# Kernel tuning notes

Measured on AMD Instinct MI355X. Metric: run time of the kernel, lower is better.

## Reference

```python
import jax, jax.numpy as jnp
import numpy as np

IN_CH = 512
HID = 512
SCALE = 1.0 / np.sqrt(16.0)  # hard-coded 16**0.5 in source, not sqrt(hidden)


def setup_inputs() -> dict:
    key = jax.random.key(0)
    ks = jax.random.split(key, 9)
    B, T = 8, 2048
    lim = 1.0 / np.sqrt(IN_CH)
    return {
        "q": jax.random.normal(ks[0], (B, T, IN_CH), dtype=jnp.float32),
        "k": jax.random.normal(ks[1], (B, T, IN_CH), dtype=jnp.float32),
        "v": jax.random.normal(ks[2], (B, T, IN_CH), dtype=jnp.float32),
        "Wq": jax.random.uniform(ks[3], (IN_CH, HID), jnp.float32, -lim, lim),
        "bq": jax.random.uniform(ks[4], (HID,), jnp.float32, -lim, lim),
        "Wk": jax.random.uniform(ks[5], (IN_CH, HID), jnp.float32, -lim, lim),
        "bk": jax.random.uniform(ks[6], (HID,), jnp.float32, -lim, lim),
        "Wv": jax.random.uniform(ks[7], (IN_CH, HID), jnp.float32, -lim, lim),
        "bv": jax.random.uniform(ks[8], (HID,), jnp.float32, -lim, lim),
    }


def reference(q, k, v, Wq, bq, Wk, bk, Wv, bv):
    # Linear projections: [B,T,F] @ [F,H] + [H]
    query = jnp.einsum("btf,fh->bth", q, Wq) + bq
    key_p = jnp.einsum("btf,fh->bth", k, Wk) + bk
    value = jnp.einsum("btf,fh->bth", v, Wv) + bv
    # energy: [B,T,T], scaled by fixed 1/sqrt(16)
    energy = jnp.einsum("bth,bsh->bts", query, key_p) * SCALE
    attn = jax.nn.softmax(energy, axis=-1)
    # weighted sum: [B,T,H]
    return jnp.einsum("bts,bsh->bth", attn, value)
```

## Files before the change

### kernel.cpp

```cpp
#include <hip/hip_runtime.h>
#include <stdint.h>

typedef __bf16 bf16;
typedef bf16 bf16x8 __attribute__((ext_vector_type(8)));
typedef float f32x4 __attribute__((ext_vector_type(4)));

#define MFMA(a, b, c) __builtin_amdgcn_mfma_f32_16x16x32_bf16(a, b, c, 0, 0, 0)

#define SCALE_L2E 0.3606737602222409f
#define M0 16.0f

#define WAITVM(N) asm volatile("s_waitcnt vmcnt(" #N ")" ::: "memory")
#define WAITLGKM0 asm volatile("s_waitcnt lgkmcnt(0)" ::: "memory")
#define SBAR __builtin_amdgcn_s_barrier()
#define SCHEDB __builtin_amdgcn_sched_barrier(0)
#define PRIO(x) __builtin_amdgcn_s_setprio(x)

__device__ __forceinline__ void gload_lds16(const void* g, void* l) {
  __builtin_amdgcn_global_load_lds(
      (const __attribute__((address_space(1))) uint32_t*)g,
      (__attribute__((address_space(3))) uint32_t*)l, 16, 0, 0);
}

__global__ void k_wtrans(const float* __restrict__ Wq, const float* __restrict__ Wk,
                         const float* __restrict__ Wv, bf16* __restrict__ Wt) {
  __shared__ float tile[32][33];
  int x = threadIdx.x, y = threadIdx.y;
  int k0 = blockIdx.x * 32, n0 = blockIdx.y * 32, z = blockIdx.z;
  const float* W = (z == 0) ? Wq : (z == 1) ? Wk : Wv;
  for (int j = 0; j < 4; j++)
    tile[y + 8 * j][x] = W[(size_t)(k0 + y + 8 * j) * 512 + n0 + x];
  __syncthreads();
  bf16* o = Wt + (size_t)z * 262144;
  for (int j = 0; j < 4; j++)
    o[(size_t)(n0 + y + 8 * j) * 512 + k0 + x] = (bf16)tile[x][y + 8 * j];
}

__global__ __launch_bounds__(256, 3) void k_proj(
    const float* __restrict__ q, const float* __restrict__ k, const float* __restrict__ v,
    const bf16* __restrict__ Wt, const float* __restrict__ bq, const float* __restrict__ bk,
    const float* __restrict__ bv, bf16* __restrict__ Qp, bf16* __restrict__ Kp,
    bf16* __restrict__ Vtp) {
  int z = blockIdx.z;
  const float* A = (z == 0) ? q : (z == 1) ? k : v;
  const float* bias = (z == 0) ? bq : (z == 1) ? bk : bv;
  const bf16* Bw = Wt + (size_t)z * 262144;

  int m0 = blockIdx.x * 128, n0 = blockIdx.y * 128;
  __shared__ __align__(16) char smem[49152];
  bf16* As = (bf16*)smem;
  bf16* Bs = (bf16*)(smem + 16384);
  bf16* Ts = (bf16*)smem;

  int tid = threadIdx.x;
  int wave = tid >> 6, lane = tid & 63, qr = lane & 15, quad = lane >> 4;
  int wm = (wave >> 1) * 64, wn = (wave & 1) * 64;

  f32x4 acc[4][4];
  for (int mi = 0; mi < 4; mi++)
    for (int ni = 0; ni < 4; ni++) acc[mi][ni] = (f32x4){0.f, 0.f, 0.f, 0.f};

  float4 rxE[4], ryE[4];
  float4 rxO[4], ryO[4];

  auto issueA = [&](int kk, float4 (&rx)[4], float4 (&ry)[4]) {
#pragma unroll
    for (int i = 0; i < 4; i++) {
      int ch = i * 256 + tid, row = ch >> 3, c = ch & 7;
      const float4* src = (const float4*)(A + (size_t)(m0 + row) * 512 + kk + c * 8);
      rx[i] = src[0];
      ry[i] = src[1];
    }
    SCHEDB;
  };

  auto issueB = [&](int kk, int buf) {
#pragma unroll
    for (int i = 0; i < 4; i++) {
      int ch = i * 256 + tid, row = ch >> 3, c = ch & 7, cs = c ^ (row & 7);
      gload_lds16(Bw + (size_t)(n0 + row) * 512 + kk + cs * 8, &Bs[buf * 8192 + ch * 8]);
    }
    SCHEDB;
  };

  auto writeA = [&](float4 (&rx)[4], float4 (&ry)[4]) {
#pragma unroll
    for (int i = 0; i < 4; i++) {
      int ch = i * 256 + tid, row = ch >> 3, c = ch & 7, cs = c ^ (row & 7);
      bf16x8 t;
      t[0] = (bf16)rx[i].x; t[1] = (bf16)rx[i].y; t[2] = (bf16)rx[i].z; t[3] = (bf16)rx[i].w;
      t[4] = (bf16)ry[i].x; t[5] = (bf16)ry[i].y; t[6] = (bf16)ry[i].z; t[7] = (bf16)ry[i].w;
      *(bf16x8*)&As[row * 64 + cs * 8] = t;
    }
  };

  auto compute = [&](int buf) {
    bf16* Bb = &Bs[buf * 8192];
#pragma unroll
    for (int h = 0; h < 2; h++) {
      bf16x8 af[4], bfv[4];
#pragma unroll
      for (int mi = 0; mi < 4; mi++) {
        int rr = wm + mi * 16 + qr;
        int cc = (h * 4 + quad) ^ (rr & 7);
        af[mi] = *(bf16x8*)&As[rr * 64 + cc * 8];
      }
#pragma unroll
      for (int ni = 0; ni < 4; ni++) {
        int rr = wn + ni * 16 + qr;
        int cc = (h * 4 + quad) ^ (rr & 7);
        bfv[ni] = *(bf16x8*)&Bb[rr * 64 + cc * 8];
      }
#pragma unroll
      for (int mi = 0; mi < 4; mi++)
#pragma unroll
        for (int ni = 0; ni < 4; ni++) acc[mi][ni] = MFMA(af[mi], bfv[ni], acc[mi][ni]);
    }
  };

  issueA(0, rxE, ryE);
  issueB(0, 0);
  issueA(64, rxO, ryO);

#pragma unroll
  for (int t = 0; t < 8; t += 2) {
    writeA(rxE, ryE);
    issueB((t + 1) * 64, 1);
    if (t < 6) issueA((t + 2) * 64, rxE, ryE);
    if (t < 6) { WAITVM(20); } else { WAITVM(12); }
    WAITLGKM0;
    SBAR;
    SCHEDB;
    compute(0);
    SBAR;

    int u = t + 1;
    writeA(rxO, ryO);
    if (u < 7) issueB((u + 1) * 64, 0);
    if (u < 6) issueA((u + 2) * 64, rxO, ryO);
    if (u < 6) { WAITVM(20); } else if (u < 7) { WAITVM(12); } else { WAITVM(0); }
    WAITLGKM0;
    SBAR;
    SCHEDB;
    compute(1);
    SBAR;
  }

  if (z == 2) {
    for (int ni = 0; ni < 4; ni++) {
      int hcol = wn + ni * 16 + qr;
      float bz = bias[n0 + hcol];
      for (int mi = 0; mi < 4; mi++) {
        int tl = wm + mi * 16 + quad * 4;
        bf16 tmp[4];
        for (int r = 0; r < 4; r++) tmp[r] = (bf16)(acc[mi][ni][r] + bz);
        *(uint64_t*)&Ts[hcol * 136 + tl] = *(uint64_t*)tmp;
      }
    }
    __syncthreads();
    int bb = m0 >> 11, t0l = m0 & 2047;
    for (int i = 0; i < 8; i++) {
      int ch = i * 256 + tid;
      int row = ch >> 4, c = ch & 15;
      *(bf16x8*)(Vtp + (size_t)(bb * 512 + n0 + row) * 2048 + t0l + c * 8) =
          *(bf16x8*)&Ts[row * 136 + c * 8];
    }
  } else {
    bf16* C = (z == 0) ? Qp : Kp;
    float sc = (z == 0) ? SCALE_L2E : 1.0f;
    for (int ni = 0; ni < 4; ni++) {
      int col = n0 + wn + ni * 16 + qr;
      float bz = bias[col];
      for (int mi = 0; mi < 4; mi++) {
        int rbase = m0 + wm + mi * 16 + quad * 4;
        for (int r = 0; r < 4; r++)
          C[(size_t)(rbase + r) * 512 + col] = (bf16)((acc[mi][ni][r] + bz) * sc);
      }
    }
  }
}

__global__ __launch_bounds__(512, 1) void k_qk(const bf16* __restrict__ Qp,
                                               const bf16* __restrict__ Kp,
                                               bf16* __restrict__ P,
                                               float* __restrict__ Lpart) {
  __shared__ __align__(16) bf16 S[65536];
  int id = blockIdx.x;
  int b = id & 7, j = id >> 3;
  int mx = j & 7, ny = j >> 3;
  const bf16* A = Qp + (size_t)b * 2048 * 512;
  const bf16* B = Kp + (size_t)b * 2048 * 512;
  bf16* Pb = P + (size_t)b * 2048 * 2048;
  int m0 = mx * 256, n0 = ny * 256;
  int tid = threadIdx.x;
  int wave = tid >> 6, lane = tid & 63, qr = lane & 15, quad = lane >> 4;
  int wm = wave >> 2, wn = wave & 3;

  f32x4 acc[8][4];
  for (int mi = 0; mi < 8; mi++)
    for (int ni = 0; ni < 4; ni++) acc[mi][ni] = (f32x4){0.f, 0.f, 0.f, 0.f};

  auto stageAj = [&](int t, int s, int jj) {
    int kk = t * 64;
    bf16* As_ = S + s * 16384;
    int ch = jj * 512 + tid, row = ch >> 3, c = ch & 7, cs = c ^ (row & 7);
    gload_lds16(A + (size_t)(m0 + row) * 512 + kk + cs * 8, As_ + ch * 8);
  };
  auto stage = [&](int t, int s) {
    int kk = t * 64;
    bf16* Bs_ = S + 32768 + s * 16384;
#pragma unroll
    for (int jj = 0; jj < 4; jj++) {
      int ch = jj * 512 + tid, row = ch >> 3, c = ch & 7, cs = c ^ (row & 7);
      gload_lds16(B + (size_t)(n0 + row) * 512 + kk + cs * 8, Bs_ + ch * 8);
    }
    stageAj(t, s, 0);
    stageAj(t, s, 2);
    stageAj(t, s, 1);
    stageAj(t, s, 3);
  };

  stage(0, 0);
  stage(1, 1);

  for (int t = 0; t < 8; t++) {
    int cur = t & 1;
    bf16* As_ = S + cur * 16384;
    bf16* Bs_ = S + 32768 + cur * 16384;

    if (t < 7) { WAITVM(10); } else { WAITVM(2); }
    SBAR;
    bf16x8 aF[4][2], bF[4][2];
#pragma unroll
    for (int mi = 0; mi < 4; mi++)
#pragma unroll
      for (int kk = 0; kk < 2; kk++) {
        int row = wm * 128 + mi * 16 + qr;
        aF[mi][kk] = *(bf16x8*)&As_[row * 64 + ((kk * 4 + quad) ^ (row & 7)) * 8];
      }
#pragma unroll
    for (int ni = 0; ni < 4; ni++)
#pragma unroll
      for (int kk = 0; kk < 2; kk++) {
        int row = wn * 64 + ni * 16 + qr;
        bF[ni][kk] = *(bf16x8*)&Bs_[row * 64 + ((kk * 4 + quad) ^ (row & 7)) * 8];
      }
    WAITLGKM0;
    SCHEDB;
    PRIO(1);
#pragma unroll
    for (int kk = 0; kk < 2; kk++)
#pragma unroll
      for (int mi = 0; mi < 4; mi++)
#pragma unroll
        for (int ni = 0; ni < 4; ni++)
          acc[mi][ni] = MFMA(aF[mi][kk], bF[ni][kk], acc[mi][ni]);
    PRIO(0);

    if (t < 7) { WAITVM(8); } else { WAITVM(0); }
    SBAR;
#pragma unroll
    for (int mi = 0; mi < 4; mi++)
#pragma unroll
      for (int kk = 0; kk < 2; kk++) {
        int row = wm * 128 + 64 + mi * 16 + qr;
        aF[mi][kk] = *(bf16x8*)&As_[row * 64 + ((kk * 4 + quad) ^ (row & 7)) * 8];
      }
    WAITLGKM0;
    SBAR;
    if (t < 6) stage(t + 2, cur);
    SCHEDB;
    PRIO(1);
#pragma unroll
    for (int kk = 0; kk < 2; kk++)
#pragma unroll
      for (int mi = 0; mi < 4; mi++)
#pragma unroll
        for (int ni = 0; ni < 4; ni++)
          acc[4 + mi][ni] = MFMA(aF[mi][kk], bF[ni][kk], acc[4 + mi][ni]);
    PRIO(0);
  }

  int slice = ny * 4 + wn;
  float* Lp = Lpart + (size_t)slice * 16384 + b * 2048;
#pragma unroll
  for (int mi = 0; mi < 8; mi++) {
    int rowb = m0 + wm * 128 + mi * 16 + quad * 4;
#pragma unroll
    for (int r = 0; r < 4; r++) {
      float s = 0.f;
      bf16* prow = Pb + (size_t)(rowb + r) * 2048 + n0 + wn * 64 + qr;
#pragma unroll
      for (int ni = 0; ni < 4; ni++) {
        float e = exp2f(acc[mi][ni][r] - M0);
        prow[ni * 16] = (bf16)e;
        s += e;
      }
      s += __shfl_xor(s, 1);
      s += __shfl_xor(s, 2);
      s += __shfl_xor(s, 4);
      s += __shfl_xor(s, 8);
      if (qr == 0) Lp[rowb + r] = s;
    }
  }
}

__global__ __launch_bounds__(512, 1) void k_pv(const bf16* __restrict__ P,
                                               const bf16* __restrict__ Vtp,
                                               const float* __restrict__ Lpart,
                                               float* __restrict__ out) {
  __shared__ __align__(16) bf16 S[49152];
  int id = blockIdx.x;
  int b = id & 7, j = id >> 3;
  int mx = j & 7, ny = j >> 3;
  const bf16* A = P + (size_t)b * 2048 * 2048;
  const bf16* B = Vtp + (size_t)b * 512 * 2048;
  int m0 = mx * 256, n0 = ny * 128;
  int tid = threadIdx.x;
  int wave = tid >> 6, lane = tid & 63, qr = lane & 15, quad = lane >> 4;
  int wmi = wave >> 1, wni = wave & 1;

  float linv_own = 0.f;
  if (tid < 256) {
    float s = 0.f;
    for (int jj = 0; jj < 32; jj++) s += Lpart[(size_t)jj * 16384 + b * 2048 + m0 + tid];
    linv_own = 1.0f / s;
  }

  f32x4 acc[4][4];
  for (int mi = 0; mi < 4; mi++)
    for (int ni = 0; ni < 4; ni++) acc[mi][ni] = (f32x4){0.f, 0.f, 0.f, 0.f};

  auto stage = [&](int t, int s) {
    int kk = t * 64;
    bf16* As_ = S + s * 16384;
    bf16* Bs_ = S + 32768 + s * 8192;
#pragma unroll
    for (int jj = 0; jj < 4; jj++) {
      int ch = jj * 512 + tid, row = ch >> 3, c = ch & 7, cs = c ^ (row & 7);
      gload_lds16(A + (size_t)(m0 + row) * 2048 + kk + cs * 8, As_ + ch * 8);
    }
#pragma unroll
    for (int jj = 0; jj < 2; jj++) {
      int ch = jj * 512 + tid, row = ch >> 3, c = ch & 7, cs = c ^ (row & 7);
      gload_lds16(B + (size_t)(n0 + row) * 2048 + kk + cs * 8, Bs_ + ch * 8);
    }
  };

  stage(0, 0);
  stage(1, 1);

  for (int t = 0; t < 32; t++) {
    int cur = t & 1;
    bf16* As_ = S + cur * 16384;
    bf16* Bs_ = S + 32768 + cur * 8192;

    if (t < 31) { WAITVM(6); } else { WAITVM(0); }
    SBAR;
    bf16x8 aF[4][2], bF[4][2];
#pragma unroll
    for (int mi = 0; mi < 4; mi++)
#pragma unroll
      for (int kk = 0; kk < 2; kk++) {
        int row = wmi * 64 + mi * 16 + qr;
        aF[mi][kk] = *(bf16x8*)&As_[row * 64 + ((kk * 4 + quad) ^ (row & 7)) * 8];
      }
#pragma unroll
    for (int ni = 0; ni < 4; ni++)
#pragma unroll
      for (int kk = 0; kk < 2; kk++) {
        int row = wni * 64 + ni * 16 + qr;
        bF[ni][kk] = *(bf16x8*)&Bs_[row * 64 + ((kk * 4 + quad) ^ (row & 7)) * 8];
      }
    WAITLGKM0;
    SBAR;
    if (t < 30) stage(t + 2, cur);
    SCHEDB;
    PRIO(1);
#pragma unroll
    for (int kk = 0; kk < 2; kk++)
#pragma unroll
      for (int mi = 0; mi < 4; mi++)
#pragma unroll
        for (int ni = 0; ni < 4; ni++)
          acc[mi][ni] = MFMA(aF[mi][kk], bF[ni][kk], acc[mi][ni]);
    PRIO(0);
  }

  WAITLGKM0;
  SBAR;
  float* Linv_s = (float*)S;
  if (tid < 256) Linv_s[tid] = linv_own;
  SBAR;

#pragma unroll
  for (int mi = 0; mi < 4; mi++) {
    int rowl = wmi * 64 + mi * 16 + quad * 4;
    float linv[4];
    for (int r = 0; r < 4; r++) linv[r] = Linv_s[rowl + r];
#pragma unroll
    for (int ni = 0; ni < 4; ni++) {
      int col = n0 + wni * 64 + ni * 16 + qr;
      float* og = out + (size_t)(b * 2048 + m0 + rowl) * 512 + col;
      for (int r = 0; r < 4; r++) og[(size_t)r * 512] = acc[mi][ni][r] * linv[r];
    }
  }
}

extern "C" void kernel_launch(void* const* d_in, const int* in_sizes, int n_in,
                              void* d_out, int out_size, void* d_ws, size_t ws_size,
                              hipStream_t stream) {
  (void)in_sizes; (void)n_in; (void)out_size; (void)ws_size;
  const float* q  = (const float*)d_in[0];
  const float* k  = (const float*)d_in[1];
  const float* v  = (const float*)d_in[2];
  const float* Wq = (const float*)d_in[3];
  const float* bq = (const float*)d_in[4];
  const float* Wk = (const float*)d_in[5];
  const float* bk = (const float*)d_in[6];
  const float* Wv = (const float*)d_in[7];
  const float* bv = (const float*)d_in[8];
  float* out = (float*)d_out;

  char* ws = (char*)d_ws;
  bf16* Wt     = (bf16*)(ws);
  bf16* Qp     = (bf16*)(ws + 1572864);
  bf16* Kp     = (bf16*)(ws + 18350080);
  bf16* Vtp    = (bf16*)(ws + 35127296);
  bf16* P      = (bf16*)(ws + 51904512);
  float* Lpart = (float*)(ws + 119013376);

  k_wtrans<<<dim3(16, 16, 3), dim3(32, 8, 1), 0, stream>>>(Wq, Wk, Wv, Wt);
  k_proj<<<dim3(128, 4, 3), 256, 0, stream>>>(q, k, v, Wt, bq, bk, bv, Qp, Kp, Vtp);
  k_qk<<<512, 512, 0, stream>>>(Qp, Kp, P, Lpart);
  k_pv<<<256, 512, 0, stream>>>(P, Vtp, Lpart, out);
}
```

Baseline: 261.6 us.

## Widen Q/K projection tiles to full hidden width, split V projection

The Q and K projections move into a new kernel where each 512-thread block computes a 128x512 output tile. Each fp32 input row tile is then loaded and converted to bf16 once, instead of once per 128-wide column block. Weight tiles are double-buffered in 144KB of dynamic LDS. The V projection, with its transposed output, stays in the old 128x128 kernel launched separately. The cost is one block per CU, heavy LDS use and an extra kernel launch.

```diff
diff --git a/kernel.cpp b/kernel.cpp
--- a/kernel.cpp
+++ b/kernel.cpp
@@ -36,15 +36,132 @@
     o[(size_t)(n0 + y + 8 * j) * 512 + k0 + x] = (bf16)tile[x][y + 8 * j];
 }
 
-__global__ __launch_bounds__(256, 3) void k_proj(
-    const float* __restrict__ q, const float* __restrict__ k, const float* __restrict__ v,
-    const bf16* __restrict__ Wt, const float* __restrict__ bq, const float* __restrict__ bk,
-    const float* __restrict__ bv, bf16* __restrict__ Qp, bf16* __restrict__ Kp,
-    bf16* __restrict__ Vtp) {
-  int z = blockIdx.z;
-  const float* A = (z == 0) ? q : (z == 1) ? k : v;
-  const float* bias = (z == 0) ? bq : (z == 1) ? bk : bv;
+__global__ __launch_bounds__(512, 1) void k_proj2(
+    const float* __restrict__ q, const float* __restrict__ k,
+    const bf16* __restrict__ Wt, const float* __restrict__ bq,
+    const float* __restrict__ bk, bf16* __restrict__ Qp, bf16* __restrict__ Kp) {
+  int z = blockIdx.y;
+  const float* A = (z == 0) ? q : k;
+  const float* bias = (z == 0) ? bq : bk;
   const bf16* Bw = Wt + (size_t)z * 262144;
+  bf16* C = (z == 0) ? Qp : Kp;
+  float sc = (z == 0) ? SCALE_L2E : 1.0f;
+
+  int m0 = blockIdx.x * 128;
+  extern __shared__ __align__(16) char smem[];
+  bf16* As = (bf16*)smem;
+  bf16* Bs = (bf16*)(smem + 16384);
+
+  int tid = threadIdx.x;
+  int wave = tid >> 6, lane = tid & 63, qr = lane & 15, quad = lane >> 4;
+  int wm2 = wave >> 2, wn4 = wave & 3;
+
+  f32x4 acc[4][8];
+  for (int mi = 0; mi < 4; mi++)
+    for (int ni = 0; ni < 8; ni++) acc[mi][ni] = (f32x4){0.f, 0.f, 0.f, 0.f};
+
+  float4 rxE[2], ryE[2];
+  float4 rxO[2], ryO[2];
+
+  auto issueA = [&](int kk, float4 (&rx)[2], float4 (&ry)[2]) {
+#pragma unroll
+    for (int i = 0; i < 2; i++) {
+      int ch = i * 512 + tid, row = ch >> 3, c = ch & 7;
+      const float4* src = (const float4*)(A + (size_t)(m0 + row) * 512 + kk + c * 8);
+      rx[i] = src[0];
+      ry[i] = src[1];
+    }
+    SCHEDB;
+  };
+
+  auto issueB = [&](int kk, int buf) {
+#pragma unroll
+    for (int j = 0; j < 8; j++) {
+      int ch = j * 512 + tid, row = ch >> 3, c = ch & 7, cs = c ^ (row & 7);
+      gload_lds16(Bw + (size_t)row * 512 + kk + cs * 8, &Bs[buf * 32768 + ch * 8]);
+    }
+    SCHEDB;
+  };
+
+  auto writeA = [&](float4 (&rx)[2], float4 (&ry)[2]) {
+#pragma unroll
+    for (int i = 0; i < 2; i++) {
+      int ch = i * 512 + tid, row = ch >> 3, c = ch & 7, cs = c ^ (row & 7);
+      bf16x8 t;
+      t[0] = (bf16)rx[i].x; t[1] = (bf16)rx[i].y; t[2] = (bf16)rx[i].z; t[3] = (bf16)rx[i].w;
+      t[4] = (bf16)ry[i].x; t[5] = (bf16)ry[i].y; t[6] = (bf16)ry[i].z; t[7] = (bf16)ry[i].w;
+      *(bf16x8*)&As[row * 64 + cs * 8] = t;
+    }
+  };
+
+  auto compute = [&](int buf) {
+    bf16* Bb = &Bs[buf * 32768];
+#pragma unroll
+    for (int kk = 0; kk < 2; kk++) {
+      bf16x8 af[4];
+#pragma unroll
+      for (int mi = 0; mi < 4; mi++) {
+        int rr = wm2 * 64 + mi * 16 + qr;
+        af[mi] = *(bf16x8*)&As[rr * 64 + (((kk * 4 + quad)) ^ (rr & 7)) * 8];
+      }
+#pragma unroll
+      for (int ni = 0; ni < 8; ni++) {
+        int rr = wn4 * 128 + ni * 16 + qr;
+        bf16x8 bfv = *(bf16x8*)&Bb[rr * 64 + (((kk * 4 + quad)) ^ (rr & 7)) * 8];
+#pragma unroll
+        for (int mi = 0; mi < 4; mi++) acc[mi][ni] = MFMA(af[mi], bfv, acc[mi][ni]);
+      }
+    }
+  };
+
+  issueA(0, rxE, ryE);
+  issueB(0, 0);
+  issueA(64, rxO, ryO);
+
+#pragma unroll
+  for (int t = 0; t < 8; t += 2) {
+    writeA(rxE, ryE);
+    issueB((t + 1) * 64, 1);
+    if (t < 6) issueA((t + 2) * 64, rxE, ryE);
+    if (t < 6) { WAITVM(16); } else { WAITVM(12); }
+    WAITLGKM0;
+    SBAR;
+    SCHEDB;
+    compute(0);
+    SBAR;
+
+    int u = t + 1;
+    writeA(rxO, ryO);
+    if (u < 7) issueB((u + 1) * 64, 0);
+    if (u < 6) issueA((u + 2) * 64, rxO, ryO);
+    if (u < 6) { WAITVM(16); } else { WAITVM(0); }
+    WAITLGKM0;
+    SBAR;
+    SCHEDB;
+    compute(1);
+    SBAR;
+  }
+
+#pragma unroll
+  for (int ni = 0; ni < 8; ni++) {
+    int col = wn4 * 128 + ni * 16 + qr;
+    float bz = bias[col];
+#pragma unroll
+    for (int mi = 0; mi < 4; mi++) {
+      int grb = m0 + wm2 * 64 + mi * 16 + quad * 4;
+#pragma unroll
+      for (int r = 0; r < 4; r++)
+        C[(size_t)(grb + r) * 512 + col] = (bf16)((acc[mi][ni][r] + bz) * sc);
+    }
+  }
+}
+
+__global__ __launch_bounds__(256, 3) void k_projV(
+    const float* __restrict__ v, const bf16* __restrict__ Wt,
+    const float* __restrict__ bv, bf16* __restrict__ Vtp) {
+  const float* A = v;
+  const float* bias = bv;
+  const bf16* Bw = Wt + (size_t)2 * 262144;
 
   int m0 = blockIdx.x * 128, n0 = blockIdx.y * 128;
   __shared__ __align__(16) char smem[49152];
@@ -146,37 +263,23 @@
     SBAR;
   }
 
-  if (z == 2) {
-    for (int ni = 0; ni < 4; ni++) {
-      int hcol = wn + ni * 16 + qr;
-      float bz = bias[n0 + hcol];
-      for (int mi = 0; mi < 4; mi++) {
-        int tl = wm + mi * 16 + quad * 4;
-        bf16 tmp[4];
-        for (int r = 0; r < 4; r++) tmp[r] = (bf16)(acc[mi][ni][r] + bz);
-        *(uint64_t*)&Ts[hcol * 136 + tl] = *(uint64_t*)tmp;
-      }
-    }
-    __syncthreads();
-    int bb = m0 >> 11, t0l = m0 & 2047;
-    for (int i = 0; i < 8; i++) {
-      int ch = i * 256 + tid;
-      int row = ch >> 4, c = ch & 15;
-      *(bf16x8*)(Vtp + (size_t)(bb * 512 + n0 + row) * 2048 + t0l + c * 8) =
-          *(bf16x8*)&Ts[row * 136 + c * 8];
-    }
-  } else {
-    bf16* C = (z == 0) ? Qp : Kp;
-    float sc = (z == 0) ? SCALE_L2E : 1.0f;
-    for (int ni = 0; ni < 4; ni++) {
-      int col = n0 + wn + ni * 16 + qr;
-      float bz = bias[col];
-      for (int mi = 0; mi < 4; mi++) {
-        int rbase = m0 + wm + mi * 16 + quad * 4;
-        for (int r = 0; r < 4; r++)
-          C[(size_t)(rbase + r) * 512 + col] = (bf16)((acc[mi][ni][r] + bz) * sc);
-      }
-    }
+  for (int ni = 0; ni < 4; ni++) {
+    int hcol = wn + ni * 16 + qr;
+    float bz = bias[n0 + hcol];
+    for (int mi = 0; mi < 4; mi++) {
+      int tl = wm + mi * 16 + quad * 4;
+      bf16 tmp[4];
+      for (int r = 0; r < 4; r++) tmp[r] = (bf16)(acc[mi][ni][r] + bz);
+      *(uint64_t*)&Ts[hcol * 136 + tl] = *(uint64_t*)tmp;
+    }
+  }
+  __syncthreads();
+  int bb = m0 >> 11, t0l = m0 & 2047;
+  for (int i = 0; i < 8; i++) {
+    int ch = i * 256 + tid;
+    int row = ch >> 4, c = ch & 15;
+    *(bf16x8*)(Vtp + (size_t)(bb * 512 + n0 + row) * 2048 + t0l + c * 8) =
+        *(bf16x8*)&Ts[row * 136 + c * 8];
   }
 }
 
@@ -431,7 +534,8 @@
   float* Lpart = (float*)(ws + 119013376);
 
   k_wtrans<<<dim3(16, 16, 3), dim3(32, 8, 1), 0, stream>>>(Wq, Wk, Wv, Wt);
-  k_proj<<<dim3(128, 4, 3), 256, 0, stream>>>(q, k, v, Wt, bq, bk, bv, Qp, Kp, Vtp);
+  k_proj2<<<dim3(128, 2), 512, 147456, stream>>>(q, k, Wt, bq, bk, Qp, Kp);
+  k_projV<<<dim3(128, 4), 256, 0, stream>>>(v, Wt, bv, Vtp);
   k_qk<<<512, 512, 0, stream>>>(Qp, Kp, P, Lpart);
   k_pv<<<256, 512, 0, stream>>>(P, Vtp, Lpart, out);
 }
```

After: 259.3 us. Within noise of the previous version (-0.9%).
